# Performance work log

Measured on AMD Instinct MI355X. Metric: run time of the kernel, lower is better.

## Reference

```python
import jax, jax.numpy as jnp
import numpy as np

D_MODEL = 1024
N_HEADS = 16
DEPTH = D_MODEL // N_HEADS


def setup_inputs() -> dict:
    key = jax.random.key(0)
    ks = jax.random.split(key, 11)
    B, S = 2, 2048
    scale = 1.0 / np.sqrt(D_MODEL)
    inp = {
        "Q": jax.random.normal(ks[0], (B, S, D_MODEL), dtype=jnp.float32),
        "K": jax.random.normal(ks[1], (B, S, D_MODEL), dtype=jnp.float32),
        "V": jax.random.normal(ks[2], (B, S, D_MODEL), dtype=jnp.float32),
        "Wq": jax.random.normal(ks[3], (D_MODEL, D_MODEL), dtype=jnp.float32) * scale,
        "bq": jnp.zeros((D_MODEL,), dtype=jnp.float32),
        "Wk": jax.random.normal(ks[4], (D_MODEL, D_MODEL), dtype=jnp.float32) * scale,
        "bk": jnp.zeros((D_MODEL,), dtype=jnp.float32),
        "Wv": jax.random.normal(ks[5], (D_MODEL, D_MODEL), dtype=jnp.float32) * scale,
        "bv": jnp.zeros((D_MODEL,), dtype=jnp.float32),
        "Wo": jax.random.normal(ks[6], (D_MODEL, D_MODEL), dtype=jnp.float32) * scale,
        "bo": jnp.zeros((D_MODEL,), dtype=jnp.float32),
    }
    return inp


def reference(Q, K, V, Wq, bq, Wk, bk, Wv, bv, Wo, bo):
    B, S, _ = Q.shape
    # Linear projections (torch Linear: x @ W.T + b)
    q = Q @ Wq.T + bq
    k = K @ Wk.T + bk
    v = V @ Wv.T + bv
    # split heads: [B, S, H, depth] -> [B, H, S, depth]
    q = q.reshape(B, S, N_HEADS, DEPTH).transpose(0, 2, 1, 3)
    k = k.reshape(B, S, N_HEADS, DEPTH).transpose(0, 2, 1, 3)
    v = v.reshape(B, S, N_HEADS, DEPTH).transpose(0, 2, 1, 3)
    # scaled dot-product attention, full [B,H,S,S] scores as in the original
    scores = jnp.einsum("bhqd,bhkd->bhqk", q, k) / jnp.sqrt(jnp.float32(DEPTH))
    attn = jax.nn.softmax(scores, axis=-1)
    out = jnp.einsum("bhqk,bhkd->bhqd", attn, v)
    # combine heads
    out = out.transpose(0, 2, 1, 3).reshape(B, S, D_MODEL)
    return out @ Wo.T + bo
```

## Files before the change

### kernel.cpp

```cpp
#include <hip/hip_runtime.h>


typedef unsigned short u16;
typedef unsigned int   u32;
typedef __attribute__((ext_vector_type(8)))  __bf16 bf16x8;
typedef __attribute__((ext_vector_type(8)))  u16    u16x8;
typedef __attribute__((ext_vector_type(4)))  u32    u32x4;
typedef __attribute__((ext_vector_type(4)))  float  f32x4;
typedef __attribute__((ext_vector_type(16))) float  f32x16;

#define MFMA16(a,b,c) __builtin_amdgcn_mfma_f32_16x16x32_bf16((a),(b),(c),0,0,0)
#define MFMA32(a,b,c) __builtin_amdgcn_mfma_f32_32x32x16_bf16((a),(b),(c),0,0,0)

__device__ __forceinline__ u16 f2bf(float f) {
    unsigned int u = __float_as_uint(f);
    return (u16)((u + 0x7FFF + ((u >> 16) & 1)) >> 16);
}
__device__ __forceinline__ u32 pack2(float a, float b) {
    return (u32)f2bf(a) | ((u32)f2bf(b) << 16);
}
__device__ __forceinline__ void gl2lds16(const void* g, void* l) {
    __builtin_amdgcn_global_load_lds((const __attribute__((address_space(1))) unsigned int*)g,
                                     (__attribute__((address_space(3))) unsigned int*)l, 16, 0, 0);
}

__global__ __launch_bounds__(256)
void cvt_all(const float* __restrict__ Q, const float* __restrict__ K, const float* __restrict__ V,
             const float* __restrict__ W0, const float* __restrict__ W1,
             const float* __restrict__ W2, const float* __restrict__ W3,
             u16* __restrict__ oq, u16* __restrict__ ok, u16* __restrict__ ov,
             u16* __restrict__ o0, u16* __restrict__ o1, u16* __restrict__ o2, u16* __restrict__ o3)
{
    const int z = blockIdx.y;
    if (z >= 3 && blockIdx.x >= 512) return;
    const float* s; u16* d;
    switch (z) {
        case 0: s = Q;  d = oq; break;
        case 1: s = K;  d = ok; break;
        case 2: s = V;  d = ov; break;
        case 3: s = W0; d = o0; break;
        case 4: s = W1; d = o1; break;
        case 5: s = W2; d = o2; break;
        default: s = W3; d = o3; break;
    }
    size_t i = ((size_t)blockIdx.x * 256 + threadIdx.x) * 8;
    f32x4 lo = *(const f32x4*)(s + i), hi = *(const f32x4*)(s + i + 4);
    u16x8 v;
    #pragma unroll
    for (int t = 0; t < 4; t++) { v[t] = f2bf(lo[t]); v[4 + t] = f2bf(hi[t]); }
    *(u16x8*)(d + i) = v;
}

template<int LAYOUT, int OUTF32, int TM>
__device__ __forceinline__ void gemm_body(const u16* __restrict__ A, const u16* __restrict__ W,
                                          const float* __restrict__ bias, void* __restrict__ outv,
                                          u16* S, int m0, int n0)
{
    constexpr int MI = TM / 32;
    u16* As = S;
    u16* Bs = S + TM * 32;
    const int tid  = threadIdx.x;
    const int wave = tid >> 6, lane = tid & 63;
    const int quad = lane >> 4, l16 = lane & 15;
    const int wr = (wave >> 1) * (TM / 2), wc = (wave & 1) * 64;

    const int sa = quad ^ (((wr + l16) >> 1) & 3);
    const int sb = quad ^ (((wc + l16) >> 1) & 3);

    f32x4 acc[MI][4] = {};

    for (int k0 = 0; k0 < 1024; k0 += 32) {
        __syncthreads();
        #pragma unroll
        for (int t = 0; t < TM / 64; t++) {
            int idx = t * 256 + tid;
            int r = idx >> 2, cc = idx & 3;
            gl2lds16(A + (size_t)(m0 + r) * 1024 + k0 + ((cc ^ ((r >> 1) & 3)) * 8), As + idx * 8);
        }
        #pragma unroll
        for (int t = 0; t < 2; t++) {
            int idx = t * 256 + tid;
            int r = idx >> 2, cc = idx & 3;
            gl2lds16(W + (size_t)(n0 + r) * 1024 + k0 + ((cc ^ ((r >> 1) & 3)) * 8), Bs + idx * 8);
        }
        __syncthreads();
        bf16x8 af[MI], bfr[4];
        #pragma unroll
        for (int i = 0; i < MI; i++)
            af[i] = *(const bf16x8*)(As + (wr + i * 16 + l16) * 32 + sa * 8);
        #pragma unroll
        for (int j = 0; j < 4; j++)
            bfr[j] = *(const bf16x8*)(Bs + (wc + j * 16 + l16) * 32 + sb * 8);
        #pragma unroll
        for (int i = 0; i < MI; i++)
            #pragma unroll
            for (int j = 0; j < 4; j++)
                acc[i][j] = MFMA16(af[i], bfr[j], acc[i][j]);
    }

    if (LAYOUT == 2) {
        float bv[4];
        #pragma unroll
        for (int j = 0; j < 4; j++) bv[j] = bias[n0 + wc + j * 16 + l16];
        #pragma unroll
        for (int i = 0; i < MI; i++)
            #pragma unroll
            for (int j = 0; j < 4; j++) {
                int gn = n0 + wc + j * 16 + l16;
                #pragma unroll
                for (int r = 0; r < 4; r++) {
                    int gm = m0 + wr + i * 16 + quad * 4 + r;
                    ((float*)outv)[(size_t)gm * 1024 + gn] = acc[i][j][r] + bv[j];
                }
            }
    } else {
        float bv[4], bm[MI][4];
        if (LAYOUT == 0) {
            #pragma unroll
            for (int j = 0; j < 4; j++) bv[j] = bias[n0 + wc + j * 16 + l16];
        } else {
            #pragma unroll
            for (int i = 0; i < MI; i++)
                #pragma unroll
                for (int r = 0; r < 4; r++) bm[i][r] = bias[m0 + wr + i * 16 + quad * 4 + r];
        }
        __syncthreads();
        u16* WR = S + wave * (16 * 68);
        #pragma unroll
        for (int i = 0; i < MI; i++) {
            #pragma unroll
            for (int j = 0; j < 4; j++)
                #pragma unroll
                for (int r = 0; r < 4; r++) {
                    float v = acc[i][j][r] + (LAYOUT == 0 ? bv[j] : bm[i][r]);
                    WR[(quad * 4 + r) * 68 + j * 16 + l16] = f2bf(v);
                }
            int gm0 = m0 + wr + i * 16, gn0 = n0 + wc;
            size_t gb;
            if (LAYOUT == 0) gb = (((size_t)(gm0 >> 11) * 16 + (gn0 >> 6)) * 2048 + (gm0 & 2047)) * 64;
            else             gb = (((size_t)(gn0 >> 11) * 16 + (gm0 >> 6)) * 64 + (gm0 & 63)) * 2048 + (gn0 & 2047);
            #pragma unroll
            for (int st = 0; st < 2; st++) {
                int chunk = st * 64 + lane;
                int row = chunk >> 3, c8 = chunk & 7;
                u16x8 v = *(const u16x8*)(WR + row * 68 + c8 * 8);
                size_t ga = (LAYOUT == 0) ? gb + row * 64 + c8 * 8 : gb + (size_t)row * 2048 + c8 * 8;
                *(u16x8*)((u16*)outv + ga) = v;
            }
        }
    }
}

__global__ __launch_bounds__(256, 3)
void gemm_qkv(const u16* __restrict__ Qb, const u16* __restrict__ Kb, const u16* __restrict__ Vb,
              const u16* __restrict__ Wq, const u16* __restrict__ Wk, const u16* __restrict__ Wv,
              const float* __restrict__ bq, const float* __restrict__ bk, const float* __restrict__ bv,
              u16* __restrict__ qh, u16* __restrict__ kh, u16* __restrict__ vt)
{
    __shared__ __align__(16) u16 S[128 * 64];
    const int z = blockIdx.z;
    if (z < 2) {
        gemm_body<0, 0, 128>(z == 0 ? Qb : Kb, z == 0 ? Wq : Wk, z == 0 ? bq : bk,
                             z == 0 ? qh : kh, S, blockIdx.y * 128, blockIdx.x * 128);
    } else {
        gemm_body<3, 0, 128>(Wv, Vb, bv, vt, S, blockIdx.x * 128, blockIdx.y * 128);
    }
}

__global__ __launch_bounds__(256, 2)
void gemm_o(const u16* __restrict__ A, const u16* __restrict__ W,
            const float* __restrict__ bias, float* __restrict__ out)
{
    __shared__ __align__(16) u16 S[64 * 32 + 128 * 32];
    gemm_body<2, 1, 64>(A, W, bias, out, S, blockIdx.y * 64, blockIdx.x * 128);
}

__global__ __launch_bounds__(256, 2)
void attn_fused(const u16* __restrict__ qh, const u16* __restrict__ kh,
                const u16* __restrict__ vt, u16* __restrict__ out)
{
    __shared__ __align__(16) u16 Ks[256 * 64];
    __shared__ __align__(16) u16 Vs[64 * 256];

    const int tid  = threadIdx.x;
    const int wave = tid >> 6, lane = tid & 63;
    const int l31 = lane & 31, h = lane >> 5;
    const int q0 = blockIdx.x * 128;
    const int hh = blockIdx.y, b = blockIdx.z;

    const size_t head = (size_t)(b * 16 + hh);
    const u16* qh_h = qh + head * (2048 * 64);
    const u16* kh_h = kh + head * (2048 * 64);
    const u16* vt_h = vt + head * (64 * 2048);

    bf16x8 qf[4];
    #pragma unroll
    for (int ks = 0; ks < 4; ks++)
        qf[ks] = *(const bf16x8*)(qh_h + (size_t)(q0 + wave * 32 + l31) * 64 + ks * 16 + h * 8);

    f32x16 oacc[2] = {};
    float lp = 0.0f;
    const float cst = 0.18033688011112042f;

    for (int kt = 0; kt < 8; kt++) {
        const int kv0 = kt * 256;
        __syncthreads();
        #pragma unroll
        for (int it = 0; it < 8; it++) {
            int idx = it * 256 + tid;
            int kr = idx >> 3, kc = idx & 7;
            gl2lds16(kh_h + (size_t)(kv0 + kr) * 64 + ((kc ^ (kr & 7)) * 8), Ks + idx * 8);
            int vr = idx >> 5, vc = idx & 31;
            gl2lds16(vt_h + (size_t)vr * 2048 + kv0 + ((vc ^ (vr & 15)) * 8), Vs + idx * 8);
        }
        __syncthreads();

        #pragma unroll
        for (int mt = 0; mt < 8; mt++) {
            f32x16 sacc = {};
            #pragma unroll
            for (int ks = 0; ks < 4; ks++) {
                int row = mt * 32 + l31;
                bf16x8 kf = *(const bf16x8*)(Ks + row * 64 + (((ks * 2 + h) ^ (l31 & 7)) * 8));
                sacc = MFMA32(kf, qf[ks], sacc);
            }
            float pv[16];
            #pragma unroll
            for (int r = 0; r < 16; r++) {
                pv[r] = __builtin_amdgcn_exp2f(sacc[r] * cst);
                lp += pv[r];
            }
            u32 P[4][2];
            #pragma unroll
            for (int g = 0; g < 4; g++) {
                P[g][0] = pack2(pv[g * 4 + 0], pv[g * 4 + 1]);
                P[g][1] = pack2(pv[g * 4 + 2], pv[g * 4 + 3]);
            }
            #pragma unroll
            for (int c16 = 0; c16 < 2; c16++) {
                u32 x0 = P[2 * c16][0], y0 = P[2 * c16 + 1][0];
                u32 x1 = P[2 * c16][1], y1 = P[2 * c16 + 1][1];
                asm volatile("v_permlane32_swap_b32 %0, %1" : "+v"(x0), "+v"(y0));
                asm volatile("v_permlane32_swap_b32 %0, %1" : "+v"(x1), "+v"(y1));
                u32x4 bw = {x0, x1, y0, y1};
                bf16x8 pB = __builtin_bit_cast(bf16x8, bw);
                int c = mt * 4 + c16 * 2 + h;
                #pragma unroll
                for (int dt = 0; dt < 2; dt++) {
                    int d = dt * 32 + l31;
                    bf16x8 vf = *(const bf16x8*)(Vs + d * 256 + ((c ^ (l31 & 15)) * 8));
                    oacc[dt] = MFMA32(vf, pB, oacc[dt]);
                }
            }
        }
    }

    lp += __shfl_xor(lp, 32);
    float inv = 1.0f / lp;

    size_t ob = ((size_t)(b * 2048 + q0 + wave * 32 + l31)) * 1024 + hh * 64;
    #pragma unroll
    for (int dt = 0; dt < 2; dt++)
        #pragma unroll
        for (int g = 0; g < 4; g++) {
            int d0 = dt * 32 + 8 * g + 4 * h;
            *(u32*)((u16*)out + ob + d0)     = pack2(oacc[dt][g * 4 + 0] * inv, oacc[dt][g * 4 + 1] * inv);
            *(u32*)((u16*)out + ob + d0 + 2) = pack2(oacc[dt][g * 4 + 2] * inv, oacc[dt][g * 4 + 3] * inv);
        }
}

extern "C" void kernel_launch(void* const* d_in, const int* in_sizes, int n_in,
                              void* d_out, int out_size, void* d_ws, size_t ws_size,
                              hipStream_t stream)
{
    const float* Q   = (const float*)d_in[0];
    const float* Kin = (const float*)d_in[1];
    const float* V   = (const float*)d_in[2];
    const float* Wq  = (const float*)d_in[3];
    const float* bq  = (const float*)d_in[4];
    const float* Wk  = (const float*)d_in[5];
    const float* bk  = (const float*)d_in[6];
    const float* Wv  = (const float*)d_in[7];
    const float* bv  = (const float*)d_in[8];
    const float* Wo  = (const float*)d_in[9];
    const float* bo  = (const float*)d_in[10];

    const size_t TS = (size_t)2 * 2048 * 1024;
    const size_t WS = (size_t)1024 * 1024;
    u16* Qb  = (u16*)d_ws;
    u16* Kb  = Qb + TS;
    u16* Vb  = Kb + TS;
    u16* qh  = Vb + TS;
    u16* kh  = qh + TS;
    u16* vt  = kh + TS;
    u16* Wqb = vt + TS;
    u16* Wkb = Wqb + WS;
    u16* Wvb = Wkb + WS;
    u16* Wob = Wvb + WS;
    u16* at  = Qb;

    cvt_all<<<dim3(2048, 7), 256, 0, stream>>>(Q, Kin, V, Wq, Wk, Wv, Wo,
                                               Qb, Kb, Vb, Wqb, Wkb, Wvb, Wob);
    gemm_qkv<<<dim3(8, 32, 3), 256, 0, stream>>>(Qb, Kb, Vb, Wqb, Wkb, Wvb, bq, bk, bv, qh, kh, vt);
    attn_fused<<<dim3(16, 16, 2), 256, 0, stream>>>(qh, kh, vt, at);
    gemm_o<<<dim3(8, 64), 256, 0, stream>>>(at, Wob, bo, (float*)d_out);
}
```

Measured before the change: 223.4 us.

## Fold softmax scale into Q projection, use hardware bf16 pack and MFMA row-sum

The softmax scale (1/sqrt(depth)·log2e) is moved into the Q projection epilogue, which removes a multiply per score in the attention loop. Software bf16 rounding is replaced with the v_cvt_pk_bf16_f32 instruction. The softmax denominator is now accumulated by an extra MFMA against a ones vector, using the same bf16-rounded P that feeds the PV product, instead of scalar adds and a shuffle. Together these cut VALU work in the exp-bound inner loop, at the cost of one extra MFMA per P block and an extra bf16 rounding of the prescaled Q.

```diff
diff --git a/kernel.cpp b/kernel.cpp
--- a/kernel.cpp
+++ b/kernel.cpp
@@ -16,8 +16,10 @@
     unsigned int u = __float_as_uint(f);
     return (u16)((u + 0x7FFF + ((u >> 16) & 1)) >> 16);
 }
-__device__ __forceinline__ u32 pack2(float a, float b) {
-    return (u32)f2bf(a) | ((u32)f2bf(b) << 16);
+__device__ __forceinline__ u32 cvtpk(float a, float b) {
+    u32 d;
+    asm("v_cvt_pk_bf16_f32 %0, %1, %2" : "=v"(d) : "v"(a), "v"(b));
+    return d;
 }
 __device__ __forceinline__ void gl2lds16(const void* g, void* l) {
     __builtin_amdgcn_global_load_lds((const __attribute__((address_space(1))) unsigned int*)g,
@@ -54,7 +56,7 @@
 template<int LAYOUT, int OUTF32, int TM>
 __device__ __forceinline__ void gemm_body(const u16* __restrict__ A, const u16* __restrict__ W,
                                           const float* __restrict__ bias, void* __restrict__ outv,
-                                          u16* S, int m0, int n0)
+                                          u16* S, int m0, int n0, float scale)
 {
     constexpr int MI = TM / 32;
     u16* As = S;
@@ -132,7 +134,7 @@
             for (int j = 0; j < 4; j++)
                 #pragma unroll
                 for (int r = 0; r < 4; r++) {
-                    float v = acc[i][j][r] + (LAYOUT == 0 ? bv[j] : bm[i][r]);
+                    float v = (acc[i][j][r] + (LAYOUT == 0 ? bv[j] : bm[i][r])) * scale;
                     WR[(quad * 4 + r) * 68 + j * 16 + l16] = f2bf(v);
                 }
             int gm0 = m0 + wr + i * 16, gn0 = n0 + wc;
@@ -151,6 +153,8 @@
     }
 }
 
+#define CST 0.18033688011112042f
+
 __global__ __launch_bounds__(256, 3)
 void gemm_qkv(const u16* __restrict__ Qb, const u16* __restrict__ Kb, const u16* __restrict__ Vb,
               const u16* __restrict__ Wq, const u16* __restrict__ Wk, const u16* __restrict__ Wv,
@@ -161,9 +165,10 @@
     const int z = blockIdx.z;
     if (z < 2) {
         gemm_body<0, 0, 128>(z == 0 ? Qb : Kb, z == 0 ? Wq : Wk, z == 0 ? bq : bk,
-                             z == 0 ? qh : kh, S, blockIdx.y * 128, blockIdx.x * 128);
+                             z == 0 ? qh : kh, S, blockIdx.y * 128, blockIdx.x * 128,
+                             z == 0 ? CST : 1.0f);
     } else {
-        gemm_body<3, 0, 128>(Wv, Vb, bv, vt, S, blockIdx.x * 128, blockIdx.y * 128);
+        gemm_body<3, 0, 128>(Wv, Vb, bv, vt, S, blockIdx.x * 128, blockIdx.y * 128, 1.0f);
     }
 }
 
@@ -172,7 +177,7 @@
             const float* __restrict__ bias, float* __restrict__ out)
 {
     __shared__ __align__(16) u16 S[64 * 32 + 128 * 32];
-    gemm_body<2, 1, 64>(A, W, bias, out, S, blockIdx.y * 64, blockIdx.x * 128);
+    gemm_body<2, 1, 64>(A, W, bias, out, S, blockIdx.y * 64, blockIdx.x * 128, 1.0f);
 }
 
 __global__ __launch_bounds__(256, 2)
@@ -198,9 +203,12 @@
     for (int ks = 0; ks < 4; ks++)
         qf[ks] = *(const bf16x8*)(qh_h + (size_t)(q0 + wave * 32 + l31) * 64 + ks * 16 + h * 8);
 
+    const u32 one2 = 0x3F803F80u;
+    const u32x4 onesw = {one2, one2, one2, one2};
+    const bf16x8 onesf = __builtin_bit_cast(bf16x8, onesw);
+
     f32x16 oacc[2] = {};
-    float lp = 0.0f;
-    const float cst = 0.18033688011112042f;
+    f32x16 lacc = {};
 
     for (int kt = 0; kt < 8; kt++) {
         const int kv0 = kt * 256;
@@ -224,17 +232,13 @@
                 bf16x8 kf = *(const bf16x8*)(Ks + row * 64 + (((ks * 2 + h) ^ (l31 & 7)) * 8));
                 sacc = MFMA32(kf, qf[ks], sacc);
             }
-            float pv[16];
-            #pragma unroll
-            for (int r = 0; r < 16; r++) {
-                pv[r] = __builtin_amdgcn_exp2f(sacc[r] * cst);
-                lp += pv[r];
-            }
             u32 P[4][2];
             #pragma unroll
             for (int g = 0; g < 4; g++) {
-                P[g][0] = pack2(pv[g * 4 + 0], pv[g * 4 + 1]);
-                P[g][1] = pack2(pv[g * 4 + 2], pv[g * 4 + 3]);
+                P[g][0] = cvtpk(__builtin_amdgcn_exp2f(sacc[g * 4 + 0]),
+                                __builtin_amdgcn_exp2f(sacc[g * 4 + 1]));
+                P[g][1] = cvtpk(__builtin_amdgcn_exp2f(sacc[g * 4 + 2]),
+                                __builtin_amdgcn_exp2f(sacc[g * 4 + 3]));
             }
             #pragma unroll
             for (int c16 = 0; c16 < 2; c16++) {
@@ -244,6 +248,7 @@
                 asm volatile("v_permlane32_swap_b32 %0, %1" : "+v"(x1), "+v"(y1));
                 u32x4 bw = {x0, x1, y0, y1};
                 bf16x8 pB = __builtin_bit_cast(bf16x8, bw);
+                lacc = MFMA32(onesf, pB, lacc);
                 int c = mt * 4 + c16 * 2 + h;
                 #pragma unroll
                 for (int dt = 0; dt < 2; dt++) {
@@ -255,8 +260,7 @@
         }
     }
 
-    lp += __shfl_xor(lp, 32);
-    float inv = 1.0f / lp;
+    float inv = 1.0f / lacc[0];
 
     size_t ob = ((size_t)(b * 2048 + q0 + wave * 32 + l31)) * 1024 + hh * 64;
     #pragma unroll
@@ -264,8 +268,8 @@
         #pragma unroll
         for (int g = 0; g < 4; g++) {
             int d0 = dt * 32 + 8 * g + 4 * h;
-            *(u32*)((u16*)out + ob + d0)     = pack2(oacc[dt][g * 4 + 0] * inv, oacc[dt][g * 4 + 1] * inv);
-            *(u32*)((u16*)out + ob + d0 + 2) = pack2(oacc[dt][g * 4 + 2] * inv, oacc[dt][g * 4 + 3] * inv);
+            *(u32*)((u16*)out + ob + d0)     = cvtpk(oacc[dt][g * 4 + 0] * inv, oacc[dt][g * 4 + 1] * inv);
+            *(u32*)((u16*)out + ob + d0 + 2) = cvtpk(oacc[dt][g * 4 + 2] * inv, oacc[dt][g * 4 + 3] * inv);
         }
 }
 
```

Measured after the change: 215.6 us. -3.5%, faster.
